# Kernel optimization log

Measured on AMD Instinct MI355X. Metric: run time of the kernel, lower is better.

The kernel has to match this reference:

```python
import jax, jax.numpy as jnp
import numpy as np

B, L, C, H = 4, 4096, 1024, 16


def setup_inputs() -> dict:
    key = jax.random.key(0)
    k1, k2, k3 = jax.random.split(key, 3)
    x = jax.random.normal(k1, (B, L, C), dtype=jnp.float32)
    # torch nn.Linear params: weight (out, in), bias (out,)
    W_qkv = jax.random.normal(k2, (3 * C, C), dtype=jnp.float32) * 0.02
    b_qkv = jnp.zeros((3 * C,), dtype=jnp.float32)
    W_out = jax.random.normal(k3, (C, C), dtype=jnp.float32) * 0.02
    b_out = jnp.zeros((C,), dtype=jnp.float32)
    return {"x": x, "W_qkv": W_qkv, "b_qkv": b_qkv, "W_out": W_out,
            "b_out": b_out, "num_heads": H}


def reference(x, W_qkv, b_qkv, W_out, b_out, num_heads):
    # Faithful to the source, INCLUDING its head-axis bug:
    # q,k,v stay (B, L, H, D); attention is computed over the HEAD axis
    # (H x H per token), and the final transpose(1,2).reshape scrambles
    # sequence/head layout exactly as torch does.
    b, l, c = x.shape
    h = num_heads
    d = c // h
    scale = d ** (-0.5)
    qkv = (x @ W_qkv.T + b_qkv).reshape(b, l, 3, h, d)
    q, k, v = qkv[:, :, 0], qkv[:, :, 1], qkv[:, :, 2]  # (B, L, H, D)
    # (B,L,H,D) @ (B,L,D,H) -> (B,L,H,H)
    attn = jnp.einsum('blhd,blgd->blhg', q, k) * scale
    attn = jax.nn.softmax(attn, axis=-1)
    # dropout is identity in eval mode
    out = jnp.einsum('blhg,blgd->blhd', attn, v)      # (B, L, H, D)
    out = jnp.swapaxes(out, 1, 2).reshape(b, l, c)    # torch transpose(1,2).reshape
    return out @ W_out.T + b_out
```

## Files before the change

### kernel.cpp

```cpp
#include <hip/hip_runtime.h>
#include <hip/hip_bf16.h>


typedef __attribute__((ext_vector_type(8))) short bf16x8;
typedef __attribute__((ext_vector_type(4))) float f32x4;

__device__ __forceinline__ float bf2f(unsigned short u) {
    union { unsigned int i; float f; } x;
    x.i = ((unsigned int)u) << 16;
    return x.f;
}
__device__ __forceinline__ unsigned short f2bf(float f) {
    unsigned int u = __float_as_uint(f);
    u = (u + 0x7FFFu + ((u >> 16) & 1u)) >> 16;
    return (unsigned short)u;
}

#define VMCNT4() asm volatile("s_waitcnt vmcnt(4)" ::: "memory")
#define VMCNT0() asm volatile("s_waitcnt vmcnt(0)" ::: "memory")
#define LGKM0()  asm volatile("s_waitcnt lgkmcnt(0)" ::: "memory")
#define BAR()    __builtin_amdgcn_s_barrier()

__global__ __launch_bounds__(256) void cast_f32_bf16(const float* __restrict__ in,
                                                     unsigned short* __restrict__ out,
                                                     int n4) {
    int i = blockIdx.x * blockDim.x + threadIdx.x;
    int stride = gridDim.x * blockDim.x;
    for (; i < n4; i += stride) {
        float4 v = ((const float4*)in)[i];
        ushort4 o;
        o.x = f2bf(v.x); o.y = f2bf(v.y); o.z = f2bf(v.z); o.w = f2bf(v.w);
        ((ushort4*)out)[i] = o;
    }
}

template<int OUTF32>
__global__ __launch_bounds__(512, 2) void gemm256(const unsigned short* __restrict__ A,
                                                  const unsigned short* __restrict__ B,
                                                  const float* __restrict__ bias,
                                                  unsigned short* __restrict__ Cb,
                                                  float* __restrict__ Cf,
                                                  int M, int N, int K, int NXT) {
    __shared__ __align__(16) unsigned short lds[2][2][2][8192];

    const int tid  = threadIdx.x;
    const int lane = tid & 63;
    const int wave = tid >> 6;
    const int wr = wave >> 2;
    const int wc = wave & 3;
    const int fr = lane & 15;
    const int fq = lane >> 4;
    const int frx = fr & 7;

    const int nwg  = gridDim.x;
    const int orig = blockIdx.x;
    const int wg   = (orig & 7) * (nwg >> 3) + (orig >> 3);
    const int tileM = (wg / NXT) * 256;
    const int tileN = (wg % NXT) * 256;

    const int r8  = tid >> 3;
    const int jsw = (tid & 7) ^ (r8 & 7);
    const unsigned short* Ap = A;
    const unsigned short* Bp = B;

#define STAGE(nb, OPp, HH, ktt) do {                                                   \
    const unsigned short* gb = (OPp) ? Bp : Ap;                                        \
    const int rb = ((OPp) ? tileN : tileM) + (HH) * 128 + r8;                          \
    const unsigned short* s0 = gb + (size_t)rb * K + (ktt) * 64 + jsw * 8;             \
    unsigned short* d0 = &lds[nb][OPp][HH][tid * 8];                                   \
    __builtin_amdgcn_global_load_lds((const __attribute__((address_space(1))) void*)s0,\
        (__attribute__((address_space(3))) void*)d0, 16, 0, 0);                        \
    __builtin_amdgcn_global_load_lds(                                                  \
        (const __attribute__((address_space(1))) void*)(s0 + (size_t)64 * K),          \
        (__attribute__((address_space(3))) void*)(d0 + 4096), 16, 0, 0);               \
} while (0)

#define QUAD_READ(h, g) do {                                                           \
    _Pragma("unroll") for (int i2 = 0; i2 < 4; ++i2) {                                 \
        const int ar = (wr * 64 + i2 * 16 + fr) * 64;                                  \
        af[i2][0] = *(const bf16x8*)&lds[cur][0][h][ar + ((fq ^ frx) << 3)];           \
        af[i2][1] = *(const bf16x8*)&lds[cur][0][h][ar + (((4 + fq) ^ frx) << 3)];     \
    }                                                                                  \
    _Pragma("unroll") for (int j2 = 0; j2 < 2; ++j2) {                                 \
        const int br = (wc * 32 + j2 * 16 + fr) * 64;                                  \
        bfr[j2][0] = *(const bf16x8*)&lds[cur][1][g][br + ((fq ^ frx) << 3)];          \
        bfr[j2][1] = *(const bf16x8*)&lds[cur][1][g][br + (((4 + fq) ^ frx) << 3)];    \
    }                                                                                  \
} while (0)

#define QUAD_MFMA(h, g) do {                                                           \
    __builtin_amdgcn_s_setprio(1);                                                     \
    _Pragma("unroll") for (int i2 = 0; i2 < 4; ++i2)                                   \
    _Pragma("unroll") for (int j2 = 0; j2 < 2; ++j2) {                                 \
        acc[(h)*4+i2][(g)*2+j2] = __builtin_amdgcn_mfma_f32_16x16x32_bf16(             \
            af[i2][0], bfr[j2][0], acc[(h)*4+i2][(g)*2+j2], 0, 0, 0);                  \
        acc[(h)*4+i2][(g)*2+j2] = __builtin_amdgcn_mfma_f32_16x16x32_bf16(             \
            af[i2][1], bfr[j2][1], acc[(h)*4+i2][(g)*2+j2], 0, 0, 0);                  \
    }                                                                                  \
    __builtin_amdgcn_s_setprio(0);                                                     \
} while (0)

    f32x4 acc[8][4];
#pragma unroll
    for (int i = 0; i < 8; ++i)
#pragma unroll
        for (int j = 0; j < 4; ++j) acc[i][j] = (f32x4){0.f, 0.f, 0.f, 0.f};

    STAGE(0, 0, 0, 0);
    STAGE(0, 1, 0, 0);
    STAGE(0, 1, 1, 0);
    STAGE(0, 0, 1, 0);
    VMCNT4();
    BAR();

    const int NT = K >> 6;
    int cur = 0;
    for (int kt = 0; kt < NT - 1; ++kt) {
        const int nb = cur ^ 1;
        bf16x8 af[4][2], bfr[2][2];
        QUAD_READ(0, 0); STAGE(nb, 0, 0, kt + 1); VMCNT4(); BAR(); LGKM0(); QUAD_MFMA(0, 0);
        QUAD_READ(0, 1); STAGE(nb, 1, 0, kt + 1); VMCNT4(); BAR(); LGKM0(); QUAD_MFMA(0, 1);
        QUAD_READ(1, 0); STAGE(nb, 1, 1, kt + 1); BAR(); LGKM0(); QUAD_MFMA(1, 0);
        QUAD_READ(1, 1); STAGE(nb, 0, 1, kt + 1); VMCNT4(); BAR(); LGKM0(); QUAD_MFMA(1, 1);
        cur = nb;
    }
    VMCNT0();
    BAR();
    {
        bf16x8 af[4][2], bfr[2][2];
        QUAD_READ(0, 0); LGKM0(); QUAD_MFMA(0, 0);
        QUAD_READ(0, 1); LGKM0(); QUAD_MFMA(0, 1);
        QUAD_READ(1, 0); LGKM0(); QUAD_MFMA(1, 0);
        QUAD_READ(1, 1); LGKM0(); QUAD_MFMA(1, 1);
    }

#pragma unroll
    for (int i = 0; i < 8; ++i) {
        const int row = tileM + (i >> 2) * 128 + wr * 64 + (i & 3) * 16 + fq * 4;
#pragma unroll
        for (int j = 0; j < 4; ++j) {
            const int col = tileN + (j >> 1) * 128 + wc * 32 + (j & 1) * 16 + fr;
            const float bv = bias[col];
#pragma unroll
            for (int r = 0; r < 4; ++r) {
                const float v = acc[i][j][r] + bv;
                if (OUTF32) Cf[(size_t)(row + r) * N + col] = v;
                else        Cb[(size_t)(row + r) * N + col] = f2bf(v);
            }
        }
    }
#undef STAGE
#undef QUAD_READ
#undef QUAD_MFMA
}

__global__ __launch_bounds__(256) void attn_kernel(const unsigned short* __restrict__ qkv,
                                                   unsigned short* __restrict__ scr) {
    __shared__ __align__(16) unsigned short sbuf[4][3072];
    __shared__ float Pl[4][256];

    const int wave = threadIdx.x >> 6, lane = threadIdx.x & 63;
    const int token = blockIdx.x * 4 + wave;
    const int b = token >> 12, l = token & 4095;

    const unsigned short* src = qkv + (size_t)token * 3072;
#pragma unroll
    for (int i = 0; i < 6; ++i) {
        int off = (i * 64 + lane) * 8;
        *(bf16x8*)&sbuf[wave][off] = *(const bf16x8*)&src[off];
    }
    __syncthreads();

    const unsigned short* sq = sbuf[wave];

    float sv[4];
#pragma unroll
    for (int r = 0; r < 4; ++r) {
        const int p = r * 64 + lane;
        const int h = p >> 4, g = p & 15;
        float acc = 0.f;
#pragma unroll
        for (int d8 = 0; d8 < 8; ++d8) {
            bf16x8 qa = *(const bf16x8*)&sq[h * 64 + d8 * 8];
            bf16x8 kb = *(const bf16x8*)&sq[1024 + g * 64 + d8 * 8];
#pragma unroll
            for (int j = 0; j < 8; ++j)
                acc += bf2f((unsigned short)qa[j]) * bf2f((unsigned short)kb[j]);
        }
        sv[r] = acc * 0.125f;
    }

#pragma unroll
    for (int r = 0; r < 4; ++r) {
        float m = sv[r];
        m = fmaxf(m, __shfl_xor(m, 1));
        m = fmaxf(m, __shfl_xor(m, 2));
        m = fmaxf(m, __shfl_xor(m, 4));
        m = fmaxf(m, __shfl_xor(m, 8));
        float e = __expf(sv[r] - m);
        float s = e;
        s += __shfl_xor(s, 1);
        s += __shfl_xor(s, 2);
        s += __shfl_xor(s, 4);
        s += __shfl_xor(s, 8);
        Pl[wave][r * 64 + lane] = e / s;
    }
    __syncthreads();

    float vreg[16];
#pragma unroll
    for (int g = 0; g < 16; ++g) vreg[g] = bf2f(sq[2048 + g * 64 + lane]);

    const int q_ = l >> 4, j = l & 15;
    const size_t base = ((size_t)b * 4096 + q_) * 1024 + j * 64 + lane;
#pragma unroll
    for (int h = 0; h < 16; ++h) {
        float acc = 0.f;
#pragma unroll
        for (int g = 0; g < 16; ++g) acc += Pl[wave][h * 16 + g] * vreg[g];
        scr[base + (size_t)h * 256 * 1024] = f2bf(acc);
    }
}

extern "C" void kernel_launch(void* const* d_in, const int* in_sizes, int n_in,
                              void* d_out, int out_size, void* d_ws, size_t ws_size,
                              hipStream_t stream) {
    const float* x    = (const float*)d_in[0];
    const float* Wqkv = (const float*)d_in[1];
    const float* bqkv = (const float*)d_in[2];
    const float* Wout = (const float*)d_in[3];
    const float* bout = (const float*)d_in[4];
    float* out = (float*)d_out;

    char* ws = (char*)d_ws;
    unsigned short* xb   = (unsigned short*)(ws);
    unsigned short* wqb  = (unsigned short*)(ws + 33554432);
    unsigned short* wob  = (unsigned short*)(ws + 39845888);
    unsigned short* qkvb = (unsigned short*)(ws + 41943040);
    unsigned short* scr  = (unsigned short*)(ws + 142606336);

    cast_f32_bf16<<<2048, 256, 0, stream>>>(x,    xb,  4194304);
    cast_f32_bf16<<<512,  256, 0, stream>>>(Wqkv, wqb, 786432);
    cast_f32_bf16<<<256,  256, 0, stream>>>(Wout, wob, 262144);

    gemm256<0><<<768, 512, 0, stream>>>(xb, wqb, bqkv, qkvb, nullptr, 16384, 3072, 1024, 12);

    attn_kernel<<<4096, 256, 0, stream>>>(qkvb, scr);

    gemm256<1><<<256, 512, 0, stream>>>(scr, wob, bout, nullptr, out, 16384, 1024, 1024, 4);
}
```

Before: 211.9 us.

## Reuse GEMM register fragments across quadrants and merge cast kernels into one launch

The three f32-to-bf16 cast launches become one kernel that picks its source and destination by index range, which saves two launch gaps. In the GEMM main loop, A and B fragments now stay in registers across the four quadrant MFMA groups, so each fragment is read from LDS once per k-step instead of twice. This drops one LDS read phase and one wait per iteration, at the cost of more live VGPRs for the extra B fragments, which could pressure occupancy under launch_bounds(512,2).

Result: faster. 197.8 us (-6.6%).

```diff
diff --git a/kernel.cpp b/kernel.cpp
--- a/kernel.cpp
+++ b/kernel.cpp
@@ -21,16 +21,24 @@
 #define LGKM0()  asm volatile("s_waitcnt lgkmcnt(0)" ::: "memory")
 #define BAR()    __builtin_amdgcn_s_barrier()
 
-__global__ __launch_bounds__(256) void cast_f32_bf16(const float* __restrict__ in,
-                                                     unsigned short* __restrict__ out,
-                                                     int n4) {
-    int i = blockIdx.x * blockDim.x + threadIdx.x;
-    int stride = gridDim.x * blockDim.x;
-    for (; i < n4; i += stride) {
-        float4 v = ((const float4*)in)[i];
+__global__ __launch_bounds__(256) void cast_all(const float* __restrict__ x,
+                                                const float* __restrict__ wq,
+                                                const float* __restrict__ wo,
+                                                unsigned short* __restrict__ xb,
+                                                unsigned short* __restrict__ wqb,
+                                                unsigned short* __restrict__ wob) {
+    const size_t base = (size_t)blockIdx.x * 2048 + threadIdx.x;
+#pragma unroll
+    for (int it = 0; it < 8; ++it) {
+        size_t i = base + (size_t)it * 256;
+        const float4* s; ushort4* d; size_t off;
+        if (i < 4194304)      { s = (const float4*)x;  d = (ushort4*)xb;  off = i; }
+        else if (i < 4980736) { s = (const float4*)wq; d = (ushort4*)wqb; off = i - 4194304; }
+        else                  { s = (const float4*)wo; d = (ushort4*)wob; off = i - 4980736; }
+        float4 v = s[off];
         ushort4 o;
         o.x = f2bf(v.x); o.y = f2bf(v.y); o.z = f2bf(v.z); o.w = f2bf(v.w);
-        ((ushort4*)out)[i] = o;
+        d[off] = o;
     }
 }
 
@@ -75,27 +83,30 @@
         (__attribute__((address_space(3))) void*)(d0 + 4096), 16, 0, 0);               \
 } while (0)
 
-#define QUAD_READ(h, g) do {                                                           \
+#define READ_A(h) do {                                                                 \
     _Pragma("unroll") for (int i2 = 0; i2 < 4; ++i2) {                                 \
         const int ar = (wr * 64 + i2 * 16 + fr) * 64;                                  \
         af[i2][0] = *(const bf16x8*)&lds[cur][0][h][ar + ((fq ^ frx) << 3)];           \
         af[i2][1] = *(const bf16x8*)&lds[cur][0][h][ar + (((4 + fq) ^ frx) << 3)];     \
     }                                                                                  \
+} while (0)
+
+#define READ_B(g) do {                                                                 \
     _Pragma("unroll") for (int j2 = 0; j2 < 2; ++j2) {                                 \
         const int br = (wc * 32 + j2 * 16 + fr) * 64;                                  \
-        bfr[j2][0] = *(const bf16x8*)&lds[cur][1][g][br + ((fq ^ frx) << 3)];          \
-        bfr[j2][1] = *(const bf16x8*)&lds[cur][1][g][br + (((4 + fq) ^ frx) << 3)];    \
+        bfr[2*(g)+j2][0] = *(const bf16x8*)&lds[cur][1][g][br + ((fq ^ frx) << 3)];    \
+        bfr[2*(g)+j2][1] = *(const bf16x8*)&lds[cur][1][g][br + (((4 + fq) ^ frx) << 3)];\
     }                                                                                  \
 } while (0)
 
-#define QUAD_MFMA(h, g) do {                                                           \
+#define MFMA_Q(h, g) do {                                                              \
     __builtin_amdgcn_s_setprio(1);                                                     \
     _Pragma("unroll") for (int i2 = 0; i2 < 4; ++i2)                                   \
     _Pragma("unroll") for (int j2 = 0; j2 < 2; ++j2) {                                 \
         acc[(h)*4+i2][(g)*2+j2] = __builtin_amdgcn_mfma_f32_16x16x32_bf16(             \
-            af[i2][0], bfr[j2][0], acc[(h)*4+i2][(g)*2+j2], 0, 0, 0);                  \
+            af[i2][0], bfr[2*(g)+j2][0], acc[(h)*4+i2][(g)*2+j2], 0, 0, 0);            \
         acc[(h)*4+i2][(g)*2+j2] = __builtin_amdgcn_mfma_f32_16x16x32_bf16(             \
-            af[i2][1], bfr[j2][1], acc[(h)*4+i2][(g)*2+j2], 0, 0, 0);                  \
+            af[i2][1], bfr[2*(g)+j2][1], acc[(h)*4+i2][(g)*2+j2], 0, 0, 0);            \
     }                                                                                  \
     __builtin_amdgcn_s_setprio(0);                                                     \
 } while (0)
@@ -117,21 +128,21 @@
     int cur = 0;
     for (int kt = 0; kt < NT - 1; ++kt) {
         const int nb = cur ^ 1;
-        bf16x8 af[4][2], bfr[2][2];
-        QUAD_READ(0, 0); STAGE(nb, 0, 0, kt + 1); VMCNT4(); BAR(); LGKM0(); QUAD_MFMA(0, 0);
-        QUAD_READ(0, 1); STAGE(nb, 1, 0, kt + 1); VMCNT4(); BAR(); LGKM0(); QUAD_MFMA(0, 1);
-        QUAD_READ(1, 0); STAGE(nb, 1, 1, kt + 1); BAR(); LGKM0(); QUAD_MFMA(1, 0);
-        QUAD_READ(1, 1); STAGE(nb, 0, 1, kt + 1); VMCNT4(); BAR(); LGKM0(); QUAD_MFMA(1, 1);
+        bf16x8 af[4][2], bfr[4][2];
+        READ_A(0); READ_B(0); STAGE(nb, 0, 0, kt + 1); VMCNT4(); BAR(); LGKM0(); MFMA_Q(0, 0);
+        READ_B(1); STAGE(nb, 1, 0, kt + 1); VMCNT4(); BAR(); LGKM0(); MFMA_Q(0, 1);
+        READ_A(1); STAGE(nb, 1, 1, kt + 1); BAR(); LGKM0(); MFMA_Q(1, 0);
+        STAGE(nb, 0, 1, kt + 1); VMCNT4(); BAR(); MFMA_Q(1, 1);
         cur = nb;
     }
     VMCNT0();
     BAR();
     {
-        bf16x8 af[4][2], bfr[2][2];
-        QUAD_READ(0, 0); LGKM0(); QUAD_MFMA(0, 0);
-        QUAD_READ(0, 1); LGKM0(); QUAD_MFMA(0, 1);
-        QUAD_READ(1, 0); LGKM0(); QUAD_MFMA(1, 0);
-        QUAD_READ(1, 1); LGKM0(); QUAD_MFMA(1, 1);
+        bf16x8 af[4][2], bfr[4][2];
+        READ_A(0); READ_B(0); LGKM0(); MFMA_Q(0, 0);
+        READ_B(1);            LGKM0(); MFMA_Q(0, 1);
+        READ_A(1);            LGKM0(); MFMA_Q(1, 0);
+                                       MFMA_Q(1, 1);
     }
 
 #pragma unroll
@@ -150,8 +161,9 @@
         }
     }
 #undef STAGE
-#undef QUAD_READ
-#undef QUAD_MFMA
+#undef READ_A
+#undef READ_B
+#undef MFMA_Q
 }
 
 __global__ __launch_bounds__(256) void attn_kernel(const unsigned short* __restrict__ qkv,
@@ -239,9 +251,7 @@
     unsigned short* qkvb = (unsigned short*)(ws + 41943040);
     unsigned short* scr  = (unsigned short*)(ws + 142606336);
 
-    cast_f32_bf16<<<2048, 256, 0, stream>>>(x,    xb,  4194304);
-    cast_f32_bf16<<<512,  256, 0, stream>>>(Wqkv, wqb, 786432);
-    cast_f32_bf16<<<256,  256, 0, stream>>>(Wout, wob, 262144);
+    cast_all<<<2560, 256, 0, stream>>>(x, Wqkv, Wout, xb, wqb, wob);
 
     gemm256<0><<<768, 512, 0, stream>>>(xb, wqb, bqkv, qkvb, nullptr, 16384, 3072, 1024, 12);
 
```
